# Performance work log

Hardware: AMD Instinct MI355X
Metric: run time of the kernel (lower is better)

## Reference

```python
import jax, jax.numpy as jnp
import numpy as np

D = 256; H = 8; L = 4; P = 4; DFF = 1024
B = 4; NQ = 900
SHAPES = np.array([[100, 160], [50, 80], [25, 40], [13, 20]], dtype=np.int64)
NV = int((SHAPES[:, 0] * SHAPES[:, 1]).sum())


def setup_inputs():
    key = jax.random.key(0)
    ks = jax.random.split(key, 16)
    def w(k, shape):
        return jax.random.normal(k, shape, jnp.float32) * 0.02
    return {
        "tgt": jax.random.normal(ks[0], (B, NQ, D), jnp.float32),
        "tgt_query_pos": jax.random.normal(ks[1], (B, NQ, D), jnp.float32),
        "tgt_reference_points": jax.random.uniform(ks[2], (B, NQ, L, 2), dtype=jnp.float32),
        "memory": jax.random.normal(ks[3], (B, NV, D), jnp.float32),
        "value_proj_w": w(ks[4], (D, D)), "value_proj_b": jnp.zeros((D,), jnp.float32),
        "samp_off_w": w(ks[5], (H * L * P * 2, D)), "samp_off_b": jnp.zeros((H * L * P * 2,), jnp.float32),
        "attn_w_w": w(ks[6], (H * L * P, D)), "attn_w_b": jnp.zeros((H * L * P,), jnp.float32),
        "ca_out_w": w(ks[7], (D, D)), "ca_out_b": jnp.zeros((D,), jnp.float32),
        "ln1_g": jnp.ones((D,), jnp.float32), "ln1_b": jnp.zeros((D,), jnp.float32),
        "in_proj_w": w(ks[8], (3 * D, D)), "in_proj_b": jnp.zeros((3 * D,), jnp.float32),
        "sa_out_w": w(ks[9], (D, D)), "sa_out_b": jnp.zeros((D,), jnp.float32),
        "ln2_g": jnp.ones((D,), jnp.float32), "ln2_b": jnp.zeros((D,), jnp.float32),
        "ffn1_w": w(ks[10], (DFF, D)), "ffn1_b": jnp.zeros((DFF,), jnp.float32),
        "ffn2_w": w(ks[11], (D, DFF)), "ffn2_b": jnp.zeros((D,), jnp.float32),
        "ln3_g": jnp.ones((D,), jnp.float32), "ln3_b": jnp.zeros((D,), jnp.float32),
        "spatial_shapes": jnp.asarray(SHAPES),
    }


def layer_norm(x, g, b, eps=1e-5):
    m = x.mean(-1, keepdims=True)
    v = ((x - m) ** 2).mean(-1, keepdims=True)
    return (x - m) / jnp.sqrt(v + eps) * g + b


def ms_deform_attn(query, refp, value, shapes, Wv, bv, Wo, bo, Wa, ba, Wout, bout):
    # query [B,Nq,D], refp [B,Nq,L,2] in [0,1], value [B,NV,D]; shapes: np [L,2] (H,W)
    Bq, Nq, Dm = query.shape
    dh = Dm // H
    v = (value @ Wv.T + bv).reshape(Bq, -1, H, dh)
    off = (query @ Wo.T + bo).reshape(Bq, Nq, H, L, P, 2)
    aw = jax.nn.softmax((query @ Wa.T + ba).reshape(Bq, Nq, H, L * P), axis=-1)
    aw = aw.reshape(Bq, Nq, H, L, P)
    norm = jnp.asarray(np.stack([shapes[:, 1], shapes[:, 0]], -1), jnp.float32)  # [L,2] = (W,H)
    loc = refp[:, :, None, :, None, :] + off / norm[None, None, None, :, None, :]  # [B,Nq,H,L,P,2]
    starts = np.concatenate([[0], np.cumsum(shapes[:, 0] * shapes[:, 1])])
    acc = jnp.zeros((Bq, Nq, H, dh), query.dtype)
    for l in range(L):
        Hl, Wl = int(shapes[l, 0]), int(shapes[l, 1])
        vf = v[:, int(starts[l]):int(starts[l]) + Hl * Wl]                 # [B,HW,H,dh]
        v2 = vf.transpose(0, 2, 1, 3).reshape(Bq * H, Hl * Wl, dh)
        # grid_sample align_corners=False: pixel = loc*size - 0.5
        xl = loc[:, :, :, l, :, 0] * Wl - 0.5                              # [B,Nq,H,P]
        yl = loc[:, :, :, l, :, 1] * Hl - 0.5
        x0 = jnp.floor(xl); y0 = jnp.floor(yl)
        wx = xl - x0; wy = yl - y0
        x0i = x0.astype(jnp.int32); y0i = y0.astype(jnp.int32)
        def corner(xi, yi, wgt):
            valid = (xi >= 0) & (xi < Wl) & (yi >= 0) & (yi < Hl)
            idx = jnp.clip(yi, 0, Hl - 1) * Wl + jnp.clip(xi, 0, Wl - 1)   # [B,Nq,H,P]
            idx2 = idx.transpose(0, 2, 1, 3).reshape(Bq * H, Nq * P)
            g = jnp.take_along_axis(v2, idx2[..., None], axis=1)           # [B*H,Nq*P,dh]
            g = g.reshape(Bq, H, Nq, P, dh).transpose(0, 2, 1, 3, 4)
            return g * (wgt * valid).astype(query.dtype)[..., None]
        s = (corner(x0i, y0i, (1 - wx) * (1 - wy))
             + corner(x0i + 1, y0i, wx * (1 - wy))
             + corner(x0i, y0i + 1, (1 - wx) * wy)
             + corner(x0i + 1, y0i + 1, wx * wy))                          # [B,Nq,H,P,dh]
        acc = acc + jnp.einsum('bqhpd,bqhp->bqhd', s, aw[:, :, :, l])
    return acc.reshape(Bq, Nq, Dm) @ Wout.T + bout


def mha(q, k, v, Win, bin_, Wout, bout):
    Dm = q.shape[-1]; dh = Dm // H
    def proj(x, W, b):
        return (x @ W.T + b).reshape(x.shape[0], x.shape[1], H, dh)
    qh = proj(q, Win[:Dm], bin_[:Dm])
    kh = proj(k, Win[Dm:2 * Dm], bin_[Dm:2 * Dm])
    vh = proj(v, Win[2 * Dm:], bin_[2 * Dm:])
    att = jax.nn.softmax(jnp.einsum('bqhd,bkhd->bhqk', qh, kh) / np.sqrt(dh).astype(np.float32), axis=-1)
    o = jnp.einsum('bhqk,bkhd->bqhd', att, vh).reshape(q.shape[0], q.shape[1], Dm)
    return o @ Wout.T + bout


def _forward(tgt, tgt_query_pos, tgt_reference_points, memory,
             value_proj_w, value_proj_b, samp_off_w, samp_off_b, attn_w_w, attn_w_b,
             ca_out_w, ca_out_b, ln1_g, ln1_b, in_proj_w, in_proj_b, sa_out_w, sa_out_b,
             ln2_g, ln2_b, ffn1_w, ffn1_b, ffn2_w, ffn2_b, ln3_g, ln3_b, shapes):
    # cross (deformable) attention
    q = tgt + tgt_query_pos
    tgt2 = ms_deform_attn(q, tgt_reference_points, memory, shapes,
                          value_proj_w, value_proj_b, samp_off_w, samp_off_b,
                          attn_w_w, attn_w_b, ca_out_w, ca_out_b)
    x = layer_norm(tgt + tgt2, ln1_g, ln1_b)
    # self attention (q=k=x+pos, v=x)
    qk = x + tgt_query_pos
    x = layer_norm(x + mha(qk, qk, x, in_proj_w, in_proj_b, sa_out_w, sa_out_b), ln2_g, ln2_b)
    # FFN
    ff = jax.nn.relu(x @ ffn1_w.T + ffn1_b) @ ffn2_w.T + ffn2_b
    return layer_norm(x + ff, ln3_g, ln3_b)


def reference(tgt, tgt_query_pos, tgt_reference_points, memory,
              value_proj_w, value_proj_b, samp_off_w, samp_off_b, attn_w_w, attn_w_b,
              ca_out_w, ca_out_b, ln1_g, ln1_b, in_proj_w, in_proj_b, sa_out_w, sa_out_b,
              ln2_g, ln2_b, ffn1_w, ffn1_b, ffn2_w, ffn2_b, ln3_g, ln3_b, spatial_shapes):
    shapes = np.asarray(spatial_shapes)
    return _forward(tgt, tgt_query_pos, tgt_reference_points, memory,
                    value_proj_w, value_proj_b, samp_off_w, samp_off_b, attn_w_w, attn_w_b,
                    ca_out_w, ca_out_b, ln1_g, ln1_b, in_proj_w, in_proj_b, sa_out_w, sa_out_b,
                    ln2_g, ln2_b, ffn1_w, ffn1_b, ffn2_w, ffn2_b, ln3_g, ln3_b, shapes)
```

## Files before the change

kernel.cpp:

```cpp
#include <hip/hip_runtime.h>

constexpr int D_   = 256;
constexpr int H_   = 8;
constexpr int DH   = 32;
constexpr int L_   = 4;
constexpr int P_   = 4;
constexpr int DFF_ = 1024;
constexpr int B_   = 4;
constexpr int NQ_  = 900;
constexpr int NV_  = 21260;
constexpr int MQ   = B_ * NQ_;
constexpr int MV   = B_ * NV_;

typedef __attribute__((ext_vector_type(8))) short short8;
typedef __attribute__((ext_vector_type(4))) float f32x4;

static __device__ __forceinline__ unsigned short f2bf(float x) {
  union { float f; unsigned int u; } v;
  v.f = x;
  const unsigned int r = v.u + 0x7fffu + ((v.u >> 16) & 1u);
  return (unsigned short)(r >> 16);
}
static __device__ __forceinline__ float bf2f(unsigned short u) {
  union { unsigned int i; float f; } x;
  x.i = ((unsigned int)u) << 16;
  return x.f;
}

struct CvtArgs {
  const float* src[9];
  unsigned short* dst[9];
  int n[9];
  float scl[9];
};

__global__ __launch_bounds__(256) void cvtw(CvtArgs a) {
  const int seg = blockIdx.y;
  const int n = a.n[seg];
  const float s = a.scl[seg];
  const float* __restrict__ sp = a.src[seg];
  unsigned short* __restrict__ d = a.dst[seg];
  for (int i = (blockIdx.x * 256 + threadIdx.x) * 4; i < n;
       i += gridDim.x * 256 * 4) {
    const float4 v = *reinterpret_cast<const float4*>(&sp[i]);
    d[i + 0] = f2bf(v.x * s); d[i + 1] = f2bf(v.y * s);
    d[i + 2] = f2bf(v.z * s); d[i + 3] = f2bf(v.w * s);
  }
}

__global__ void biasprep(const float* __restrict__ bin,
                         const float* __restrict__ bo,
                         const float* __restrict__ ba,
                         float* __restrict__ bqkv, float* __restrict__ bfu) {
  const int i = threadIdx.x;
  if (i < 768) bqkv[i] = (i < 256) ? bin[i] * 0.17677669529663687f : bin[i];
  if (i < 384) bfu[i] = (i < 256) ? bo[i] : ba[i - 256];
}

template <bool ABF, bool ADD2, bool RELU, bool OUTBF>
__global__ __launch_bounds__(256) void gemm_db(
    const void* __restrict__ Ap, const float* __restrict__ A2,
    const unsigned short* __restrict__ Wbf, const float* __restrict__ bias,
    void* __restrict__ Cp, int M, int N, int K) {
  constexpr int LDR = 40;
  __shared__ unsigned short As[2][128][LDR];
  __shared__ unsigned short Bs[2][128][LDR];

  const float* Af = (const float*)Ap;
  const unsigned short* Ab = (const unsigned short*)Ap;
  float* Cf = (float*)Cp;
  unsigned short* Cb = (unsigned short*)Cp;

  const int t    = threadIdx.x;
  const int wave = t >> 6;
  const int l    = t & 63;
  const int n0   = blockIdx.x * 128;
  const int m0   = blockIdx.y * 128;
  const int wm   = (wave >> 1) * 64;
  const int wn   = (wave & 1) * 64;
  const int srow = t >> 1;
  const int sseg = (t & 1) * 16;
  const int lr   = l & 15;
  const int lk   = (l >> 4) * 8;

  const int am = m0 + srow;
  const bool aok = am < M;
  const size_t arow = (size_t)am * K;
  const size_t brow = (size_t)(n0 + srow) * K;

  f32x4 acc[4][4];
#pragma unroll
  for (int i = 0; i < 4; ++i)
#pragma unroll
    for (int j = 0; j < 4; ++j) acc[i][j] = (f32x4)0.f;

  short8 ar0, ar1, br0, br1;

  auto LOAD = [&](int k0) {
    if constexpr (ABF) {
      if (aok) {
        ar0 = *reinterpret_cast<const short8*>(&Ab[arow + k0 + sseg]);
        ar1 = *reinterpret_cast<const short8*>(&Ab[arow + k0 + sseg + 8]);
      } else {
        ar0 = (short8)(short)0; ar1 = (short8)(short)0;
      }
    } else {
      if (aok) {
        float f[16];
#pragma unroll
        for (int j = 0; j < 4; ++j) {
          const float4 av =
              *reinterpret_cast<const float4*>(&Af[arow + k0 + sseg + 4 * j]);
          f[4 * j + 0] = av.x; f[4 * j + 1] = av.y;
          f[4 * j + 2] = av.z; f[4 * j + 3] = av.w;
        }
        if constexpr (ADD2) {
#pragma unroll
          for (int j = 0; j < 4; ++j) {
            const float4 av =
                *reinterpret_cast<const float4*>(&A2[arow + k0 + sseg + 4 * j]);
            f[4 * j + 0] += av.x; f[4 * j + 1] += av.y;
            f[4 * j + 2] += av.z; f[4 * j + 3] += av.w;
          }
        }
        alignas(16) unsigned short u[16];
#pragma unroll
        for (int j = 0; j < 16; ++j) u[j] = f2bf(f[j]);
        ar0 = *reinterpret_cast<short8*>(&u[0]);
        ar1 = *reinterpret_cast<short8*>(&u[8]);
      } else {
        ar0 = (short8)(short)0; ar1 = (short8)(short)0;
      }
    }
    br0 = *reinterpret_cast<const short8*>(&Wbf[brow + k0 + sseg]);
    br1 = *reinterpret_cast<const short8*>(&Wbf[brow + k0 + sseg + 8]);
  };

  const int nt = K >> 5;
  LOAD(0);
  for (int tt = 0; tt < nt; ++tt) {
    const int cur = tt & 1;
    *reinterpret_cast<short8*>(&As[cur][srow][sseg])     = ar0;
    *reinterpret_cast<short8*>(&As[cur][srow][sseg + 8]) = ar1;
    *reinterpret_cast<short8*>(&Bs[cur][srow][sseg])     = br0;
    *reinterpret_cast<short8*>(&Bs[cur][srow][sseg + 8]) = br1;
    if (tt + 1 < nt) LOAD((tt + 1) << 5);
    __syncthreads();

    short8 af[4], bfr[4];
#pragma unroll
    for (int fi = 0; fi < 4; ++fi)
      af[fi] = *reinterpret_cast<const short8*>(&As[cur][wm + fi * 16 + lr][lk]);
#pragma unroll
    for (int fj = 0; fj < 4; ++fj)
      bfr[fj] = *reinterpret_cast<const short8*>(&Bs[cur][wn + fj * 16 + lr][lk]);

#pragma unroll
    for (int fi = 0; fi < 4; ++fi)
#pragma unroll
      for (int fj = 0; fj < 4; ++fj)
        acc[fi][fj] = __builtin_amdgcn_mfma_f32_16x16x32_bf16(
            af[fi], bfr[fj], acc[fi][fj], 0, 0, 0);
  }

  const int orow = (l >> 4) * 4;
#pragma unroll
  for (int fi = 0; fi < 4; ++fi) {
#pragma unroll
    for (int fj = 0; fj < 4; ++fj) {
      const int n = n0 + wn + fj * 16 + lr;
      const float bn = bias[n];
#pragma unroll
      for (int i = 0; i < 4; ++i) {
        const int m = m0 + wm + fi * 16 + orow + i;
        if (m < M) {
          float vv = acc[fi][fj][i] + bn;
          if (RELU) vv = fmaxf(vv, 0.f);
          if (OUTBF)
            Cb[(size_t)m * N + n] = f2bf(vv);
          else
            Cf[(size_t)m * N + n] = vv;
        }
      }
    }
  }
}

template <int K, bool ABF, bool ADD2, bool RELU, bool OUTBF>
__global__ __launch_bounds__(256) void gemm_p2(
    const void* __restrict__ Ap, const float* __restrict__ A2,
    const unsigned short* __restrict__ Wbf, const float* __restrict__ bias,
    void* __restrict__ Cp, int M, int N) {
  constexpr int LDR = 40;
  constexpr int NT = K / 32;
  __shared__ unsigned short As[2][128][LDR];
  __shared__ unsigned short Bs[2][128][LDR];

  const float* Af = (const float*)Ap;
  const unsigned short* Ab = (const unsigned short*)Ap;
  float* Cf = (float*)Cp;
  unsigned short* Cb = (unsigned short*)Cp;

  const int t    = threadIdx.x;
  const int wave = t >> 6;
  const int l    = t & 63;
  const int n0   = blockIdx.x * 128;
  const int m0   = blockIdx.y * 128;
  const int wm   = (wave >> 1) * 64;
  const int wn   = (wave & 1) * 64;
  const int srow = t >> 1;
  const int sseg = (t & 1) * 16;
  const int lr   = l & 15;
  const int lk   = (l >> 4) * 8;

  const int am = m0 + srow;
  const bool aok = am < M;
  const size_t arow = (size_t)am * K;
  const size_t brow = (size_t)(n0 + srow) * K;

  f32x4 acc[4][4];
#pragma unroll
  for (int i = 0; i < 4; ++i)
#pragma unroll
    for (int j = 0; j < 4; ++j) acc[i][j] = (f32x4)0.f;

  float  frA[16], frB[16];
  short8 abA0, abA1, abB0, abB1;
  short8 brA0, brA1, brB0, brB1;

#define LOAD_SLOT(SUF, k0)                                                     \
  do {                                                                         \
    if constexpr (ABF) {                                                       \
      if (aok) {                                                               \
        ab##SUF##0 = *reinterpret_cast<const short8*>(&Ab[arow + (k0) + sseg]);\
        ab##SUF##1 = *reinterpret_cast<const short8*>(&Ab[arow + (k0) + sseg + 8]);\
      } else {                                                                 \
        ab##SUF##0 = (short8)(short)0; ab##SUF##1 = (short8)(short)0;          \
      }                                                                        \
    } else {                                                                   \
      if (aok) {                                                               \
        _Pragma("unroll")                                                      \
        for (int j = 0; j < 4; ++j) {                                          \
          const float4 av =                                                    \
              *reinterpret_cast<const float4*>(&Af[arow + (k0) + sseg + 4 * j]);\
          fr##SUF[4 * j + 0] = av.x; fr##SUF[4 * j + 1] = av.y;                \
          fr##SUF[4 * j + 2] = av.z; fr##SUF[4 * j + 3] = av.w;                \
        }                                                                      \
        if constexpr (ADD2) {                                                  \
          _Pragma("unroll")                                                    \
          for (int j = 0; j < 4; ++j) {                                        \
            const float4 av =                                                  \
                *reinterpret_cast<const float4*>(&A2[arow + (k0) + sseg + 4 * j]);\
            fr##SUF[4 * j + 0] += av.x; fr##SUF[4 * j + 1] += av.y;            \
            fr##SUF[4 * j + 2] += av.z; fr##SUF[4 * j + 3] += av.w;            \
          }                                                                    \
        }                                                                      \
      } else {                                                                 \
        _Pragma("unroll")                                                      \
        for (int j = 0; j < 16; ++j) fr##SUF[j] = 0.f;                         \
      }                                                                        \
    }                                                                          \
    br##SUF##0 = *reinterpret_cast<const short8*>(&Wbf[brow + (k0) + sseg]);   \
    br##SUF##1 = *reinterpret_cast<const short8*>(&Wbf[brow + (k0) + sseg + 8]);\
  } while (0)

#define WRITE_SLOT(SUF, BUF)                                                   \
  do {                                                                         \
    if constexpr (ABF) {                                                       \
      *reinterpret_cast<short8*>(&As[BUF][srow][sseg])     = ab##SUF##0;       \
      *reinterpret_cast<short8*>(&As[BUF][srow][sseg + 8]) = ab##SUF##1;       \
    } else {                                                                   \
      alignas(16) unsigned short u[16];                                        \
      _Pragma("unroll")                                                        \
      for (int j = 0; j < 16; ++j) u[j] = f2bf(fr##SUF[j]);                    \
      *reinterpret_cast<short8*>(&As[BUF][srow][sseg]) =                       \
          *reinterpret_cast<short8*>(&u[0]);                                   \
      *reinterpret_cast<short8*>(&As[BUF][srow][sseg + 8]) =                   \
          *reinterpret_cast<short8*>(&u[8]);                                   \
    }                                                                          \
    *reinterpret_cast<short8*>(&Bs[BUF][srow][sseg])     = br##SUF##0;         \
    *reinterpret_cast<short8*>(&Bs[BUF][srow][sseg + 8]) = br##SUF##1;         \
  } while (0)

#define MFMA_STEP(BUF)                                                         \
  do {                                                                         \
    short8 af0 = *reinterpret_cast<const short8*>(&As[BUF][wm +  0 + lr][lk]); \
    short8 af1 = *reinterpret_cast<const short8*>(&As[BUF][wm + 16 + lr][lk]); \
    short8 af2 = *reinterpret_cast<const short8*>(&As[BUF][wm + 32 + lr][lk]); \
    short8 af3 = *reinterpret_cast<const short8*>(&As[BUF][wm + 48 + lr][lk]); \
    short8 bf0 = *reinterpret_cast<const short8*>(&Bs[BUF][wn +  0 + lr][lk]); \
    short8 bf1 = *reinterpret_cast<const short8*>(&Bs[BUF][wn + 16 + lr][lk]); \
    short8 bf2 = *reinterpret_cast<const short8*>(&Bs[BUF][wn + 32 + lr][lk]); \
    short8 bf3 = *reinterpret_cast<const short8*>(&Bs[BUF][wn + 48 + lr][lk]); \
    acc[0][0] = __builtin_amdgcn_mfma_f32_16x16x32_bf16(af0, bf0, acc[0][0], 0, 0, 0); \
    acc[0][1] = __builtin_amdgcn_mfma_f32_16x16x32_bf16(af0, bf1, acc[0][1], 0, 0, 0); \
    acc[0][2] = __builtin_amdgcn_mfma_f32_16x16x32_bf16(af0, bf2, acc[0][2], 0, 0, 0); \
    acc[0][3] = __builtin_amdgcn_mfma_f32_16x16x32_bf16(af0, bf3, acc[0][3], 0, 0, 0); \
    acc[1][0] = __builtin_amdgcn_mfma_f32_16x16x32_bf16(af1, bf0, acc[1][0], 0, 0, 0); \
    acc[1][1] = __builtin_amdgcn_mfma_f32_16x16x32_bf16(af1, bf1, acc[1][1], 0, 0, 0); \
    acc[1][2] = __builtin_amdgcn_mfma_f32_16x16x32_bf16(af1, bf2, acc[1][2], 0, 0, 0); \
    acc[1][3] = __builtin_amdgcn_mfma_f32_16x16x32_bf16(af1, bf3, acc[1][3], 0, 0, 0); \
    acc[2][0] = __builtin_amdgcn_mfma_f32_16x16x32_bf16(af2, bf0, acc[2][0], 0, 0, 0); \
    acc[2][1] = __builtin_amdgcn_mfma_f32_16x16x32_bf16(af2, bf1, acc[2][1], 0, 0, 0); \
    acc[2][2] = __builtin_amdgcn_mfma_f32_16x16x32_bf16(af2, bf2, acc[2][2], 0, 0, 0); \
    acc[2][3] = __builtin_amdgcn_mfma_f32_16x16x32_bf16(af2, bf3, acc[2][3], 0, 0, 0); \
    acc[3][0] = __builtin_amdgcn_mfma_f32_16x16x32_bf16(af3, bf0, acc[3][0], 0, 0, 0); \
    acc[3][1] = __builtin_amdgcn_mfma_f32_16x16x32_bf16(af3, bf1, acc[3][1], 0, 0, 0); \
    acc[3][2] = __builtin_amdgcn_mfma_f32_16x16x32_bf16(af3, bf2, acc[3][2], 0, 0, 0); \
    acc[3][3] = __builtin_amdgcn_mfma_f32_16x16x32_bf16(af3, bf3, acc[3][3], 0, 0, 0); \
  } while (0)

  LOAD_SLOT(A, 0);
  LOAD_SLOT(B, 32);
#pragma unroll
  for (int tt = 0; tt < NT; tt += 2) {
    WRITE_SLOT(A, 0);
    if (tt + 2 < NT) LOAD_SLOT(A, (tt + 2) * 32);
    __syncthreads();
    MFMA_STEP(0);

    WRITE_SLOT(B, 1);
    if (tt + 3 < NT) LOAD_SLOT(B, (tt + 3) * 32);
    __syncthreads();
    MFMA_STEP(1);
  }
#undef LOAD_SLOT
#undef WRITE_SLOT
#undef MFMA_STEP

  const int orow = (l >> 4) * 4;
#pragma unroll
  for (int fi = 0; fi < 4; ++fi) {
#pragma unroll
    for (int fj = 0; fj < 4; ++fj) {
      const int n = n0 + wn + fj * 16 + lr;
      const float bn = bias[n];
#pragma unroll
      for (int i = 0; i < 4; ++i) {
        const int m = m0 + wm + fi * 16 + orow + i;
        if (m < M) {
          float vv = acc[fi][fj][i] + bn;
          if (RELU) vv = fmaxf(vv, 0.f);
          if (OUTBF)
            Cb[(size_t)m * N + n] = f2bf(vv);
          else
            Cf[(size_t)m * N + n] = vv;
        }
      }
    }
  }
}

template <bool ABF, bool ADD2, bool RELU, bool OUTBF>
__global__ __launch_bounds__(256) void gemm_bres(
    const void* __restrict__ Ap, const float* __restrict__ A2,
    const unsigned short* __restrict__ Wbf, const float* __restrict__ bias,
    void* __restrict__ Cp, int M, int N, int add_nlim) {
  __shared__ unsigned short Bs[32768];
  __shared__ unsigned short As[2][64][40];

  const float* Af = (const float*)Ap;
  const unsigned short* Ab = (const unsigned short*)Ap;
  float* Cf = (float*)Cp;
  unsigned short* Cb = (unsigned short*)Cp;

  const int t    = threadIdx.x;
  const int wave = t >> 6;
  const int l    = t & 63;
  const int n0   = blockIdx.x * 128;
  const int m0   = blockIdx.y * 64;
  const int wm   = (wave >> 1) * 32;
  const int wcg  = (wave & 1) * 4;
  const int lr   = l & 15;
  const int lk8  = (l >> 4) * 8;
  const bool doadd = ADD2 && (n0 < add_nlim);

#pragma unroll
  for (int i = 0; i < 16; ++i) {
    const int e  = i * 256 + t;
    const int el = e & 63;
    const int cg = (e >> 6) & 7;
    const int st = e >> 9;
    const int row = n0 + cg * 16 + (el & 15);
    const int col = st * 32 + ((el >> 4) * 8);
    *reinterpret_cast<short8*>(&Bs[e * 8]) =
        *reinterpret_cast<const short8*>(&Wbf[(size_t)row * 256 + col]);
  }

  const int arow = t >> 2;
  const int acol = (t & 3) * 8;
  const int am   = m0 + arow;
  const bool aok = am < M;
  const size_t abase = (size_t)am * 256 + acol;

  float  fr[3][8];
  short8 br_[3];

  auto ALOAD = [&](int slot, int tt) {
    const int k0 = tt * 32;
    if constexpr (ABF) {
      br_[slot] = aok ? *reinterpret_cast<const short8*>(&Ab[abase + k0])
                      : (short8)(short)0;
    } else {
      if (aok) {
        const float4 a0 = *reinterpret_cast<const float4*>(&Af[abase + k0]);
        const float4 a1 = *reinterpret_cast<const float4*>(&Af[abase + k0 + 4]);
        fr[slot][0] = a0.x; fr[slot][1] = a0.y;
        fr[slot][2] = a0.z; fr[slot][3] = a0.w;
        fr[slot][4] = a1.x; fr[slot][5] = a1.y;
        fr[slot][6] = a1.z; fr[slot][7] = a1.w;
        if constexpr (ADD2) {
          if (doadd) {
            const float4 b0 = *reinterpret_cast<const float4*>(&A2[abase + k0]);
            const float4 b1 = *reinterpret_cast<const float4*>(&A2[abase + k0 + 4]);
            fr[slot][0] += b0.x; fr[slot][1] += b0.y;
            fr[slot][2] += b0.z; fr[slot][3] += b0.w;
            fr[slot][4] += b1.x; fr[slot][5] += b1.y;
            fr[slot][6] += b1.z; fr[slot][7] += b1.w;
          }
        }
      } else {
#pragma unroll
        for (int j = 0; j < 8; ++j) fr[slot][j] = 0.f;
      }
    }
  };
  auto AWRITE = [&](int slot, int tt) {
    if constexpr (ABF) {
      *reinterpret_cast<short8*>(&As[tt & 1][arow][acol]) = br_[slot];
    } else {
      alignas(16) unsigned short u[8];
#pragma unroll
      for (int j = 0; j < 8; ++j) u[j] = f2bf(fr[slot][j]);
      *reinterpret_cast<short8*>(&As[tt & 1][arow][acol]) =
          *reinterpret_cast<short8*>(&u[0]);
    }
  };

  f32x4 acc[2][4];
#pragma unroll
  for (int fi = 0; fi < 2; ++fi)
#pragma unroll
    for (int fj = 0; fj < 4; ++fj) acc[fi][fj] = (f32x4)0.f;

  ALOAD(0, 0); ALOAD(1, 1); ALOAD(2, 2);

#pragma unroll
  for (int tt = 0; tt < 8; ++tt) {
    AWRITE(tt % 3, tt);
    if (tt + 3 < 8) ALOAD(tt % 3, tt + 3);
    __syncthreads();

    short8 afr[2];
#pragma unroll
    for (int fi = 0; fi < 2; ++fi)
      afr[fi] = *reinterpret_cast<const short8*>(&As[tt & 1][wm + fi * 16 + lr][lk8]);

#pragma unroll
    for (int fj = 0; fj < 4; ++fj) {
      const short8 bfr = *reinterpret_cast<const short8*>(
          &Bs[(((tt * 8) + wcg + fj) * 64 + l) * 8]);
      acc[0][fj] = __builtin_amdgcn_mfma_f32_16x16x32_bf16(afr[0], bfr, acc[0][fj], 0, 0, 0);
      acc[1][fj] = __builtin_amdgcn_mfma_f32_16x16x32_bf16(afr[1], bfr, acc[1][fj], 0, 0, 0);
    }
  }

  const int or4 = (l >> 4) * 4;
#pragma unroll
  for (int fi = 0; fi < 2; ++fi) {
#pragma unroll
    for (int fj = 0; fj < 4; ++fj) {
      const int n = n0 + (wave & 1) * 64 + fj * 16 + lr;
      const float bn = bias[n];
#pragma unroll
      for (int i = 0; i < 4; ++i) {
        const int m = m0 + wm + fi * 16 + or4 + i;
        if (m < M) {
          float vv = acc[fi][fj][i] + bn;
          if (RELU) vv = fmaxf(vv, 0.f);
          if (OUTBF)
            Cb[(size_t)m * N + n] = f2bf(vv);
          else
            Cf[(size_t)m * N + n] = vv;
        }
      }
    }
  }
}

__global__ __launch_bounds__(256) void deform(const float* __restrict__ refp,
                                              const float* __restrict__ offlog,
                                              const unsigned short* __restrict__ v,
                                              unsigned int* __restrict__ accb2) {
  __shared__ float aw[2][128];
  const int t  = threadIdx.x;
  const int tq = t >> 7;
  const int tt = t & 127;
  const int bq = blockIdx.x * 2 + tq;
  const int b  = bq / NQ_;
  const int h  = tt >> 4;
  const int dd = tt & 15;

  aw[tq][tt] = offlog[(size_t)bq * 384 + 256 + tt];
  __syncthreads();
  if (t < 16) {
    const int q = t >> 3, hh = t & 7;
    float* a = &aw[q][hh * 16];
    float mx = -1e30f;
#pragma unroll
    for (int i = 0; i < 16; ++i) mx = fmaxf(mx, a[i]);
    float e[16], s = 0.f;
#pragma unroll
    for (int i = 0; i < 16; ++i) { e[i] = expf(a[i] - mx); s += e[i]; }
    const float inv = 1.f / s;
#pragma unroll
    for (int i = 0; i < 16; ++i) a[i] = e[i] * inv;
  }
  __syncthreads();

  constexpr int ST[4] = {0, 16000, 20000, 21000};
  constexpr int HL[4] = {100, 50, 25, 13};
  constexpr int WL[4] = {160, 80, 40, 20};

  float a0 = 0.f, a1 = 0.f;
#pragma unroll
  for (int l = 0; l < L_; ++l) {
    const float rx = refp[(bq * L_ + l) * 2 + 0];
    const float ry = refp[(bq * L_ + l) * 2 + 1];
    const float Wf = (float)WL[l], Hf = (float)HL[l];
    const int   Wi = WL[l], Hi = HL[l];
    const size_t vbase = (size_t)(b * NV_ + ST[l]) * D_ + h * DH + dd * 2;
#pragma unroll
    for (int p = 0; p < P_; ++p) {
      const float ox = offlog[(size_t)bq * 384 + h * 32 + l * 8 + p * 2 + 0];
      const float oy = offlog[(size_t)bq * 384 + h * 32 + l * 8 + p * 2 + 1];
      const float locx = rx + ox / Wf;
      const float locy = ry + oy / Hf;
      const float xl = locx * Wf - 0.5f;
      const float yl = locy * Hf - 0.5f;
      const float x0 = floorf(xl), y0 = floorf(yl);
      const float wx = xl - x0, wy = yl - y0;
      const int x0i = (int)x0, y0i = (int)y0;
      const float w = aw[tq][h * 16 + l * 4 + p];

      float s0 = 0.f, s1 = 0.f;
#pragma unroll
      for (int c = 0; c < 4; ++c) {
        const int xi = x0i + (c & 1);
        const int yi = y0i + (c >> 1);
        const float cw = ((c & 1) ? wx : 1.f - wx) * ((c >> 1) ? wy : 1.f - wy);
        const bool valid = (xi >= 0) && (xi < Wi) && (yi >= 0) && (yi < Hi);
        const int xc = min(max(xi, 0), Wi - 1);
        const int yc = min(max(yi, 0), Hi - 1);
        const unsigned int g2 = *reinterpret_cast<const unsigned int*>(
            &v[vbase + (size_t)(yc * Wi + xc) * D_]);
        const float g0 = bf2f((unsigned short)(g2 & 0xffffu));
        const float g1 = bf2f((unsigned short)(g2 >> 16));
        s0 += valid ? g0 * cw : 0.f;
        s1 += valid ? g1 * cw : 0.f;
      }
      a0 += w * s0;
      a1 += w * s1;
    }
  }
  const unsigned int packed =
      (unsigned int)f2bf(a0) | ((unsigned int)f2bf(a1) << 16);
  accb2[((size_t)bq * D_ + h * DH + dd * 2) >> 1] = packed;
}

constexpr int TQM  = 64;
constexpr int NQTM = (NQ_ + TQM - 1) / TQM;

__global__ __launch_bounds__(256) void mha_mfma(
    const unsigned short* __restrict__ qkvh,
    unsigned short* __restrict__ o) {
  __shared__ unsigned short Qs[64][40];
  __shared__ unsigned short Ks[64][40];
  __shared__ unsigned short Vts[32][72];
  __shared__ unsigned short Ps[64][72];

  const int bx = blockIdx.x;
  const int qt = bx % NQTM;
  const int h  = (bx / NQTM) % H_;
  const int b  = bx / (NQTM * H_);
  const int t  = threadIdx.x;
  const int wave = t >> 6;
  const int l    = t & 63;
  const int q0   = qt * TQM;
  const int wrow = wave * 16;
  const int lr   = l & 15;
  const int lkb  = (l >> 4) * 8;

  const int kr = t >> 2, kcb = (t & 3) * 8;
  const int vk = t & 63, vdb = (t >> 6) * 8;

  short8 ku, vu;
  auto LOADKV = [&](int kt) {
    const int k0 = kt * 64;
    const int nk = min(64, NQ_ - k0);
    ku = (kr < nk) ? *reinterpret_cast<const short8*>(
                         &qkvh[(size_t)(b * NQ_ + k0 + kr) * 768 + 256 + h * DH + kcb])
                   : (short8)(short)0;
    vu = (vk < nk) ? *reinterpret_cast<const short8*>(
                         &qkvh[(size_t)(b * NQ_ + k0 + vk) * 768 + 512 + h * DH + vdb])
                   : (short8)(short)0;
  };

  {
    short8 u;
    if (q0 + kr < NQ_)
      u = *reinterpret_cast<const short8*>(
          &qkvh[(size_t)(b * NQ_ + q0 + kr) * 768 + h * DH + kcb]);
    else
      u = (short8)(short)0;
    *reinterpret_cast<short8*>(&Qs[kr][kcb]) = u;
  }
  LOADKV(0);
  __syncthreads();

  const short8 qa = *reinterpret_cast<const short8*>(&Qs[wrow + lr][lkb]);

  f32x4 oacc[2];
  oacc[0] = (f32x4)0.f; oacc[1] = (f32x4)0.f;
  float m_[4] = {-1e30f, -1e30f, -1e30f, -1e30f};
  float l_[4] = {0.f, 0.f, 0.f, 0.f};

  for (int kt = 0; kt < NQTM; ++kt) {
    const int k0 = kt * 64;
    const int nk = min(64, NQ_ - k0);
    __syncthreads();

    *reinterpret_cast<short8*>(&Ks[kr][kcb]) = ku;
#pragma unroll
    for (int j = 0; j < 8; ++j) Vts[vdb + j][vk] = (unsigned short)vu[j];

    if (kt + 1 < NQTM) LOADKV(kt + 1);
    __syncthreads();

    f32x4 sacc[4];
#pragma unroll
    for (int fj = 0; fj < 4; ++fj)
      sacc[fj] = __builtin_amdgcn_mfma_f32_16x16x32_bf16(
          qa, *reinterpret_cast<const short8*>(&Ks[16 * fj + lr][lkb]),
          (f32x4)0.f, 0, 0, 0);

    bool cv[4];
#pragma unroll
    for (int fj = 0; fj < 4; ++fj) cv[fj] = (16 * fj + lr) < nk;

    float p0[4], p1[4], p2[4], p3[4], sc_[4];
#pragma unroll
    for (int i = 0; i < 4; ++i) {
      float tm = -1e30f;
      if (cv[0]) tm = fmaxf(tm, sacc[0][i]);
      if (cv[1]) tm = fmaxf(tm, sacc[1][i]);
      if (cv[2]) tm = fmaxf(tm, sacc[2][i]);
      if (cv[3]) tm = fmaxf(tm, sacc[3][i]);
      tm = fmaxf(tm, __shfl_xor(tm, 1));
      tm = fmaxf(tm, __shfl_xor(tm, 2));
      tm = fmaxf(tm, __shfl_xor(tm, 4));
      tm = fmaxf(tm, __shfl_xor(tm, 8));
      const float mn = fmaxf(m_[i], tm);
      sc_[i] = __expf(m_[i] - mn);
      m_[i] = mn;
      const float e0 = cv[0] ? __expf(sacc[0][i] - mn) : 0.f;
      const float e1 = cv[1] ? __expf(sacc[1][i] - mn) : 0.f;
      const float e2 = cv[2] ? __expf(sacc[2][i] - mn) : 0.f;
      const float e3 = cv[3] ? __expf(sacc[3][i] - mn) : 0.f;
      p0[i] = e0; p1[i] = e1; p2[i] = e2; p3[i] = e3;
      float rs = e0 + e1 + e2 + e3;
      rs += __shfl_xor(rs, 1);
      rs += __shfl_xor(rs, 2);
      rs += __shfl_xor(rs, 4);
      rs += __shfl_xor(rs, 8);
      l_[i] = l_[i] * sc_[i] + rs;
    }

#pragma unroll
    for (int i = 0; i < 4; ++i) {
      const int pr = wrow + (l >> 4) * 4 + i;
      Ps[pr][0  + lr] = f2bf(p0[i]);
      Ps[pr][16 + lr] = f2bf(p1[i]);
      Ps[pr][32 + lr] = f2bf(p2[i]);
      Ps[pr][48 + lr] = f2bf(p3[i]);
    }

    const short8 pa0 = *reinterpret_cast<const short8*>(&Ps[wrow + lr][lkb]);
    const short8 pa1 = *reinterpret_cast<const short8*>(&Ps[wrow + lr][lkb + 32]);
#pragma unroll
    for (int nt = 0; nt < 2; ++nt) {
      f32x4 c = oacc[nt];
#pragma unroll
      for (int i = 0; i < 4; ++i) c[i] *= sc_[i];
      c = __builtin_amdgcn_mfma_f32_16x16x32_bf16(
          pa0, *reinterpret_cast<const short8*>(&Vts[16 * nt + lr][lkb]), c, 0, 0, 0);
      c = __builtin_amdgcn_mfma_f32_16x16x32_bf16(
          pa1, *reinterpret_cast<const short8*>(&Vts[16 * nt + lr][lkb + 32]), c, 0, 0, 0);
      oacc[nt] = c;
    }
  }

#pragma unroll
  for (int i = 0; i < 4; ++i) {
    const int r = (l >> 4) * 4 + i;
    const int q = q0 + wrow + r;
    if (q < NQ_) {
      const float inv = 1.f / l_[i];
      o[(size_t)(b * NQ_ + q) * D_ + h * DH + 0  + lr] = f2bf(oacc[0][i] * inv);
      o[(size_t)(b * NQ_ + q) * D_ + h * DH + 16 + lr] = f2bf(oacc[1][i] * inv);
    }
  }
}

__global__ __launch_bounds__(256) void ln4(const float* __restrict__ res,
                                           const float* __restrict__ add,
                                           const float* __restrict__ g,
                                           const float* __restrict__ bt,
                                           float* __restrict__ out) {
  const int wave = threadIdx.x >> 6, lane = threadIdx.x & 63;
  const int r = blockIdx.x * 4 + wave;
  const size_t base = (size_t)r * D_ + lane * 4;
  const float4 a = *reinterpret_cast<const float4*>(&res[base]);
  const float4 bv = *reinterpret_cast<const float4*>(&add[base]);
  float4 x;
  x.x = a.x + bv.x; x.y = a.y + bv.y; x.z = a.z + bv.z; x.w = a.w + bv.w;

  float s = x.x + x.y + x.z + x.w;
#pragma unroll
  for (int off = 1; off < 64; off <<= 1) s += __shfl_xor(s, off);
  const float mean = s * (1.f / D_);

  const float dx0 = x.x - mean, dx1 = x.y - mean, dx2 = x.z - mean,
              dx3 = x.w - mean;
  float v = dx0 * dx0 + dx1 * dx1 + dx2 * dx2 + dx3 * dx3;
#pragma unroll
  for (int off = 1; off < 64; off <<= 1) v += __shfl_xor(v, off);
  const float rstd = rsqrtf(v * (1.f / D_) + 1e-5f);

  const float4 gg = *reinterpret_cast<const float4*>(&g[lane * 4]);
  const float4 bb = *reinterpret_cast<const float4*>(&bt[lane * 4]);
  float4 o;
  o.x = dx0 * rstd * gg.x + bb.x;
  o.y = dx1 * rstd * gg.y + bb.y;
  o.z = dx2 * rstd * gg.z + bb.z;
  o.w = dx3 * rstd * gg.w + bb.w;
  *reinterpret_cast<float4*>(&out[base]) = o;
}

extern "C" void kernel_launch(void* const* d_in, const int* in_sizes, int n_in,
                              void* d_out, int out_size, void* d_ws,
                              size_t ws_size, hipStream_t stream) {
  const float* tgt   = (const float*)d_in[0];
  const float* pos   = (const float*)d_in[1];
  const float* refp  = (const float*)d_in[2];
  const float* mem   = (const float*)d_in[3];
  const float* Wv    = (const float*)d_in[4];
  const float* bv    = (const float*)d_in[5];
  const float* Wo    = (const float*)d_in[6];
  const float* bo    = (const float*)d_in[7];
  const float* Wa    = (const float*)d_in[8];
  const float* ba    = (const float*)d_in[9];
  const float* Wca   = (const float*)d_in[10];
  const float* bca   = (const float*)d_in[11];
  const float* g1    = (const float*)d_in[12];
  const float* b1    = (const float*)d_in[13];
  const float* Win   = (const float*)d_in[14];
  const float* bin   = (const float*)d_in[15];
  const float* Wsa   = (const float*)d_in[16];
  const float* bsa   = (const float*)d_in[17];
  const float* g2    = (const float*)d_in[18];
  const float* b2    = (const float*)d_in[19];
  const float* W1    = (const float*)d_in[20];
  const float* bb1   = (const float*)d_in[21];
  const float* W2    = (const float*)d_in[22];
  const float* bb2   = (const float*)d_in[23];
  const float* g3    = (const float*)d_in[24];
  const float* b3    = (const float*)d_in[25];

  char* cur = (char*)d_ws;
  auto alloc = [&](size_t bytes) {
    char* p = cur;
    cur += (bytes + 255) & ~(size_t)255;
    return (void*)p;
  };
  unsigned short* v_bf    = (unsigned short*)alloc((size_t)MV * 256 * 2);
  float*          offlog  = (float*)alloc((size_t)MQ * 384 * 4);
  unsigned short* accb_bf = (unsigned short*)alloc((size_t)MQ * 256 * 2);
  float*          tmp     = (float*)alloc((size_t)MQ * 256 * 4);
  float*          x1      = (float*)alloc((size_t)MQ * 256 * 4);
  float*          x2      = (float*)alloc((size_t)MQ * 256 * 4);
  unsigned short* qkvh_bf = (unsigned short*)alloc((size_t)MQ * 768 * 2);
  unsigned short* obuf_bf = (unsigned short*)alloc((size_t)MQ * 256 * 2);
  unsigned short* h1_bf   = (unsigned short*)alloc((size_t)MQ * 1024 * 2);
  unsigned short* Wv_bf   = (unsigned short*)alloc(65536 * 2);
  unsigned short* Wfu_bf  = (unsigned short*)alloc(98304 * 2);
  unsigned short* Wca_bf  = (unsigned short*)alloc(65536 * 2);
  unsigned short* Win_bf  = (unsigned short*)alloc(196608 * 2);
  unsigned short* Wsa_bf  = (unsigned short*)alloc(65536 * 2);
  unsigned short* W1_bf   = (unsigned short*)alloc(262144 * 2);
  unsigned short* W2_bf   = (unsigned short*)alloc(262144 * 2);
  float*          biasqkv = (float*)alloc(768 * 4);
  float*          bfused  = (float*)alloc(384 * 4);

  const float qscale = 0.17677669529663687f;

  CvtArgs ca;
  ca.src[0] = Wv;            ca.dst[0] = Wv_bf;          ca.n[0] = 65536;  ca.scl[0] = 1.f;
  ca.src[1] = Wo;            ca.dst[1] = Wfu_bf;         ca.n[1] = 65536;  ca.scl[1] = 1.f;
  ca.src[2] = Wa;            ca.dst[2] = Wfu_bf + 65536; ca.n[2] = 32768;  ca.scl[2] = 1.f;
  ca.src[3] = Wca;           ca.dst[3] = Wca_bf;         ca.n[3] = 65536;  ca.scl[3] = 1.f;
  ca.src[4] = Win;           ca.dst[4] = Win_bf;         ca.n[4] = 65536;  ca.scl[4] = qscale;
  ca.src[5] = Win + 65536;   ca.dst[5] = Win_bf + 65536; ca.n[5] = 131072; ca.scl[5] = 1.f;
  ca.src[6] = Wsa;           ca.dst[6] = Wsa_bf;         ca.n[6] = 65536;  ca.scl[6] = 1.f;
  ca.src[7] = W1;            ca.dst[7] = W1_bf;          ca.n[7] = 262144; ca.scl[7] = 1.f;
  ca.src[8] = W2;            ca.dst[8] = W2_bf;          ca.n[8] = 262144; ca.scl[8] = 1.f;
  cvtw<<<dim3(64, 9), 256, 0, stream>>>(ca);
  biasprep<<<1, 768, 0, stream>>>(bin, bo, ba, biasqkv, bfused);

  const int mqb64  = (MQ + 63) / 64;
  const int mvb128 = (MV + 127) / 128;

  gemm_db<false, false, false, true><<<dim3(2, mvb128), 256, 0, stream>>>(
      mem, nullptr, Wv_bf, bv, v_bf, MV, 256, 256);
  gemm_bres<false, true, false, false><<<dim3(3, mqb64), 256, 0, stream>>>(
      tgt, pos, Wfu_bf, bfused, offlog, MQ, 384, 384);
  deform<<<MQ / 2, 256, 0, stream>>>(refp, offlog, v_bf,
                                     (unsigned int*)accb_bf);
  gemm_bres<true, false, false, false><<<dim3(2, mqb64), 256, 0, stream>>>(
      accb_bf, nullptr, Wca_bf, bca, tmp, MQ, 256, 0);
  ln4<<<MQ / 4, 256, 0, stream>>>(tgt, tmp, g1, b1, x1);
  gemm_bres<false, true, false, true><<<dim3(6, mqb64), 256, 0, stream>>>(
      x1, pos, Win_bf, biasqkv, qkvh_bf, MQ, 768, 512);
  mha_mfma<<<B_ * H_ * NQTM, 256, 0, stream>>>(qkvh_bf, obuf_bf);
  gemm_bres<true, false, false, false><<<dim3(2, mqb64), 256, 0, stream>>>(
      obuf_bf, nullptr, Wsa_bf, bsa, tmp, MQ, 256, 0);
  ln4<<<MQ / 4, 256, 0, stream>>>(x1, tmp, g2, b2, x2);
  gemm_bres<false, false, true, true><<<dim3(8, mqb64), 256, 0, stream>>>(
      x2, nullptr, W1_bf, bb1, h1_bf, MQ, 1024, 0);
  gemm_p2<1024, true, false, false, false><<<dim3(2, (MQ + 127) / 128), 256, 0, stream>>>(
      h1_bf, nullptr, W2_bf, bb2, tmp, MQ, 256);
  ln4<<<MQ / 4, 256, 0, stream>>>(x2, tmp, g3, b3, (float*)d_out);
}
```

Baseline: 201.1 us.

## Split-K FFN2 GEMM with LDS-resident weights and remap deform block order

Result: faster. 193.6 us, median of 2 (-3.7%).

```diff
diff --git a/kernel.cpp b/kernel.cpp
--- a/kernel.cpp
+++ b/kernel.cpp
@@ -162,171 +162,6 @@
         acc[fi][fj] = __builtin_amdgcn_mfma_f32_16x16x32_bf16(
             af[fi], bfr[fj], acc[fi][fj], 0, 0, 0);
   }
-
-  const int orow = (l >> 4) * 4;
-#pragma unroll
-  for (int fi = 0; fi < 4; ++fi) {
-#pragma unroll
-    for (int fj = 0; fj < 4; ++fj) {
-      const int n = n0 + wn + fj * 16 + lr;
-      const float bn = bias[n];
-#pragma unroll
-      for (int i = 0; i < 4; ++i) {
-        const int m = m0 + wm + fi * 16 + orow + i;
-        if (m < M) {
-          float vv = acc[fi][fj][i] + bn;
-          if (RELU) vv = fmaxf(vv, 0.f);
-          if (OUTBF)
-            Cb[(size_t)m * N + n] = f2bf(vv);
-          else
-            Cf[(size_t)m * N + n] = vv;
-        }
-      }
-    }
-  }
-}
-
-template <int K, bool ABF, bool ADD2, bool RELU, bool OUTBF>
-__global__ __launch_bounds__(256) void gemm_p2(
-    const void* __restrict__ Ap, const float* __restrict__ A2,
-    const unsigned short* __restrict__ Wbf, const float* __restrict__ bias,
-    void* __restrict__ Cp, int M, int N) {
-  constexpr int LDR = 40;
-  constexpr int NT = K / 32;
-  __shared__ unsigned short As[2][128][LDR];
-  __shared__ unsigned short Bs[2][128][LDR];
-
-  const float* Af = (const float*)Ap;
-  const unsigned short* Ab = (const unsigned short*)Ap;
-  float* Cf = (float*)Cp;
-  unsigned short* Cb = (unsigned short*)Cp;
-
-  const int t    = threadIdx.x;
-  const int wave = t >> 6;
-  const int l    = t & 63;
-  const int n0   = blockIdx.x * 128;
-  const int m0   = blockIdx.y * 128;
-  const int wm   = (wave >> 1) * 64;
-  const int wn   = (wave & 1) * 64;
-  const int srow = t >> 1;
-  const int sseg = (t & 1) * 16;
-  const int lr   = l & 15;
-  const int lk   = (l >> 4) * 8;
-
-  const int am = m0 + srow;
-  const bool aok = am < M;
-  const size_t arow = (size_t)am * K;
-  const size_t brow = (size_t)(n0 + srow) * K;
-
-  f32x4 acc[4][4];
-#pragma unroll
-  for (int i = 0; i < 4; ++i)
-#pragma unroll
-    for (int j = 0; j < 4; ++j) acc[i][j] = (f32x4)0.f;
-
-  float  frA[16], frB[16];
-  short8 abA0, abA1, abB0, abB1;
-  short8 brA0, brA1, brB0, brB1;
-
-#define LOAD_SLOT(SUF, k0)                                                     \
-  do {                                                                         \
-    if constexpr (ABF) {                                                       \
-      if (aok) {                                                               \
-        ab##SUF##0 = *reinterpret_cast<const short8*>(&Ab[arow + (k0) + sseg]);\
-        ab##SUF##1 = *reinterpret_cast<const short8*>(&Ab[arow + (k0) + sseg + 8]);\
-      } else {                                                                 \
-        ab##SUF##0 = (short8)(short)0; ab##SUF##1 = (short8)(short)0;          \
-      }                                                                        \
-    } else {                                                                   \
-      if (aok) {                                                               \
-        _Pragma("unroll")                                                      \
-        for (int j = 0; j < 4; ++j) {                                          \
-          const float4 av =                                                    \
-              *reinterpret_cast<const float4*>(&Af[arow + (k0) + sseg + 4 * j]);\
-          fr##SUF[4 * j + 0] = av.x; fr##SUF[4 * j + 1] = av.y;                \
-          fr##SUF[4 * j + 2] = av.z; fr##SUF[4 * j + 3] = av.w;                \
-        }                                                                      \
-        if constexpr (ADD2) {                                                  \
-          _Pragma("unroll")                                                    \
-          for (int j = 0; j < 4; ++j) {                                        \
-            const float4 av =                                                  \
-                *reinterpret_cast<const float4*>(&A2[arow + (k0) + sseg + 4 * j]);\
-            fr##SUF[4 * j + 0] += av.x; fr##SUF[4 * j + 1] += av.y;            \
-            fr##SUF[4 * j + 2] += av.z; fr##SUF[4 * j + 3] += av.w;            \
-          }                                                                    \
-        }                                                                      \
-      } else {                                                                 \
-        _Pragma("unroll")                                                      \
-        for (int j = 0; j < 16; ++j) fr##SUF[j] = 0.f;                         \
-      }                                                                        \
-    }                                                                          \
-    br##SUF##0 = *reinterpret_cast<const short8*>(&Wbf[brow + (k0) + sseg]);   \
-    br##SUF##1 = *reinterpret_cast<const short8*>(&Wbf[brow + (k0) + sseg + 8]);\
-  } while (0)
-
-#define WRITE_SLOT(SUF, BUF)                                                   \
-  do {                                                                         \
-    if constexpr (ABF) {                                                       \
-      *reinterpret_cast<short8*>(&As[BUF][srow][sseg])     = ab##SUF##0;       \
-      *reinterpret_cast<short8*>(&As[BUF][srow][sseg + 8]) = ab##SUF##1;       \
-    } else {                                                                   \
-      alignas(16) unsigned short u[16];                                        \
-      _Pragma("unroll")                                                        \
-      for (int j = 0; j < 16; ++j) u[j] = f2bf(fr##SUF[j]);                    \
-      *reinterpret_cast<short8*>(&As[BUF][srow][sseg]) =                       \
-          *reinterpret_cast<short8*>(&u[0]);                                   \
-      *reinterpret_cast<short8*>(&As[BUF][srow][sseg + 8]) =                   \
-          *reinterpret_cast<short8*>(&u[8]);                                   \
-    }                                                                          \
-    *reinterpret_cast<short8*>(&Bs[BUF][srow][sseg])     = br##SUF##0;         \
-    *reinterpret_cast<short8*>(&Bs[BUF][srow][sseg + 8]) = br##SUF##1;         \
-  } while (0)
-
-#define MFMA_STEP(BUF)                                                         \
-  do {                                                                         \
-    short8 af0 = *reinterpret_cast<const short8*>(&As[BUF][wm +  0 + lr][lk]); \
-    short8 af1 = *reinterpret_cast<const short8*>(&As[BUF][wm + 16 + lr][lk]); \
-    short8 af2 = *reinterpret_cast<const short8*>(&As[BUF][wm + 32 + lr][lk]); \
-    short8 af3 = *reinterpret_cast<const short8*>(&As[BUF][wm + 48 + lr][lk]); \
-    short8 bf0 = *reinterpret_cast<const short8*>(&Bs[BUF][wn +  0 + lr][lk]); \
-    short8 bf1 = *reinterpret_cast<const short8*>(&Bs[BUF][wn + 16 + lr][lk]); \
-    short8 bf2 = *reinterpret_cast<const short8*>(&Bs[BUF][wn + 32 + lr][lk]); \
-    short8 bf3 = *reinterpret_cast<const short8*>(&Bs[BUF][wn + 48 + lr][lk]); \
-    acc[0][0] = __builtin_amdgcn_mfma_f32_16x16x32_bf16(af0, bf0, acc[0][0], 0, 0, 0); \
-    acc[0][1] = __builtin_amdgcn_mfma_f32_16x16x32_bf16(af0, bf1, acc[0][1], 0, 0, 0); \
-    acc[0][2] = __builtin_amdgcn_mfma_f32_16x16x32_bf16(af0, bf2, acc[0][2], 0, 0, 0); \
-    acc[0][3] = __builtin_amdgcn_mfma_f32_16x16x32_bf16(af0, bf3, acc[0][3], 0, 0, 0); \
-    acc[1][0] = __builtin_amdgcn_mfma_f32_16x16x32_bf16(af1, bf0, acc[1][0], 0, 0, 0); \
-    acc[1][1] = __builtin_amdgcn_mfma_f32_16x16x32_bf16(af1, bf1, acc[1][1], 0, 0, 0); \
-    acc[1][2] = __builtin_amdgcn_mfma_f32_16x16x32_bf16(af1, bf2, acc[1][2], 0, 0, 0); \
-    acc[1][3] = __builtin_amdgcn_mfma_f32_16x16x32_bf16(af1, bf3, acc[1][3], 0, 0, 0); \
-    acc[2][0] = __builtin_amdgcn_mfma_f32_16x16x32_bf16(af2, bf0, acc[2][0], 0, 0, 0); \
-    acc[2][1] = __builtin_amdgcn_mfma_f32_16x16x32_bf16(af2, bf1, acc[2][1], 0, 0, 0); \
-    acc[2][2] = __builtin_amdgcn_mfma_f32_16x16x32_bf16(af2, bf2, acc[2][2], 0, 0, 0); \
-    acc[2][3] = __builtin_amdgcn_mfma_f32_16x16x32_bf16(af2, bf3, acc[2][3], 0, 0, 0); \
-    acc[3][0] = __builtin_amdgcn_mfma_f32_16x16x32_bf16(af3, bf0, acc[3][0], 0, 0, 0); \
-    acc[3][1] = __builtin_amdgcn_mfma_f32_16x16x32_bf16(af3, bf1, acc[3][1], 0, 0, 0); \
-    acc[3][2] = __builtin_amdgcn_mfma_f32_16x16x32_bf16(af3, bf2, acc[3][2], 0, 0, 0); \
-    acc[3][3] = __builtin_amdgcn_mfma_f32_16x16x32_bf16(af3, bf3, acc[3][3], 0, 0, 0); \
-  } while (0)
-
-  LOAD_SLOT(A, 0);
-  LOAD_SLOT(B, 32);
-#pragma unroll
-  for (int tt = 0; tt < NT; tt += 2) {
-    WRITE_SLOT(A, 0);
-    if (tt + 2 < NT) LOAD_SLOT(A, (tt + 2) * 32);
-    __syncthreads();
-    MFMA_STEP(0);
-
-    WRITE_SLOT(B, 1);
-    if (tt + 3 < NT) LOAD_SLOT(B, (tt + 3) * 32);
-    __syncthreads();
-    MFMA_STEP(1);
-  }
-#undef LOAD_SLOT
-#undef WRITE_SLOT
-#undef MFMA_STEP
 
   const int orow = (l >> 4) * 4;
 #pragma unroll
@@ -488,15 +323,126 @@
   }
 }
 
+__global__ __launch_bounds__(256) void gemm_ffn2(
+    const unsigned short* __restrict__ Ab,
+    const unsigned short* __restrict__ Wbf,
+    float* __restrict__ Cpart, int M) {
+  __shared__ unsigned short Bs[32768];
+  __shared__ unsigned short As[2][64][40];
+
+  const int t    = threadIdx.x;
+  const int wave = t >> 6;
+  const int l    = t & 63;
+  const int n0   = blockIdx.x * 128;
+  const int m0   = blockIdx.y * 64;
+  const int kz   = blockIdx.z * 256;
+  const int wm   = (wave >> 1) * 32;
+  const int wcg  = (wave & 1) * 4;
+  const int lr   = l & 15;
+  const int lk8  = (l >> 4) * 8;
+
+#pragma unroll
+  for (int i = 0; i < 16; ++i) {
+    const int e  = i * 256 + t;
+    const int el = e & 63;
+    const int cg = (e >> 6) & 7;
+    const int st = e >> 9;
+    const int row = n0 + cg * 16 + (el & 15);
+    const int col = kz + st * 32 + ((el >> 4) * 8);
+    *reinterpret_cast<short8*>(&Bs[e * 8]) =
+        *reinterpret_cast<const short8*>(&Wbf[(size_t)row * 1024 + col]);
+  }
+
+  const int arow = t >> 2;
+  const int acol = (t & 3) * 8;
+  const int am   = m0 + arow;
+  const bool aok = am < M;
+  const size_t abase = (size_t)am * 1024 + kz + acol;
+
+  short8 br_[3];
+  auto ALOAD = [&](int slot, int tt) {
+    br_[slot] = aok ? *reinterpret_cast<const short8*>(&Ab[abase + tt * 32])
+                    : (short8)(short)0;
+  };
+  auto AWRITE = [&](int slot, int tt) {
+    *reinterpret_cast<short8*>(&As[tt & 1][arow][acol]) = br_[slot];
+  };
+
+  f32x4 acc[2][4];
+#pragma unroll
+  for (int fi = 0; fi < 2; ++fi)
+#pragma unroll
+    for (int fj = 0; fj < 4; ++fj) acc[fi][fj] = (f32x4)0.f;
+
+  ALOAD(0, 0); ALOAD(1, 1); ALOAD(2, 2);
+
+#pragma unroll
+  for (int tt = 0; tt < 8; ++tt) {
+    AWRITE(tt % 3, tt);
+    if (tt + 3 < 8) ALOAD(tt % 3, tt + 3);
+    __syncthreads();
+
+    short8 afr[2];
+#pragma unroll
+    for (int fi = 0; fi < 2; ++fi)
+      afr[fi] = *reinterpret_cast<const short8*>(&As[tt & 1][wm + fi * 16 + lr][lk8]);
+
+#pragma unroll
+    for (int fj = 0; fj < 4; ++fj) {
+      const short8 bfr = *reinterpret_cast<const short8*>(
+          &Bs[(((tt * 8) + wcg + fj) * 64 + l) * 8]);
+      acc[0][fj] = __builtin_amdgcn_mfma_f32_16x16x32_bf16(afr[0], bfr, acc[0][fj], 0, 0, 0);
+      acc[1][fj] = __builtin_amdgcn_mfma_f32_16x16x32_bf16(afr[1], bfr, acc[1][fj], 0, 0, 0);
+    }
+  }
+
+  float* out = &Cpart[(size_t)blockIdx.z * M * 256];
+  const int or4 = (l >> 4) * 4;
+#pragma unroll
+  for (int fi = 0; fi < 2; ++fi) {
+#pragma unroll
+    for (int fj = 0; fj < 4; ++fj) {
+      const int n = n0 + (wave & 1) * 64 + fj * 16 + lr;
+#pragma unroll
+      for (int i = 0; i < 4; ++i) {
+        const int m = m0 + wm + fi * 16 + or4 + i;
+        if (m < M) out[(size_t)m * 256 + n] = acc[fi][fj][i];
+      }
+    }
+  }
+}
+
+__global__ __launch_bounds__(256) void reduce4(const float* __restrict__ part,
+                                               const float* __restrict__ bias,
+                                               float* __restrict__ out, int M) {
+  const size_t i = ((size_t)blockIdx.x * 256 + threadIdx.x) * 4;
+  const size_t tot = (size_t)M * 256;
+  if (i >= tot) return;
+  const int nb = (int)(i & 255);
+  float4 s = *reinterpret_cast<const float4*>(&part[i]);
+  const float4 p1 = *reinterpret_cast<const float4*>(&part[tot + i]);
+  const float4 p2 = *reinterpret_cast<const float4*>(&part[2 * tot + i]);
+  const float4 p3 = *reinterpret_cast<const float4*>(&part[3 * tot + i]);
+  const float4 bb = *reinterpret_cast<const float4*>(&bias[nb]);
+  s.x += p1.x + p2.x + p3.x + bb.x;
+  s.y += p1.y + p2.y + p3.y + bb.y;
+  s.z += p1.z + p2.z + p3.z + bb.z;
+  s.w += p1.w + p2.w + p3.w + bb.w;
+  *reinterpret_cast<float4*>(&out[i]) = s;
+}
+
 __global__ __launch_bounds__(256) void deform(const float* __restrict__ refp,
                                               const float* __restrict__ offlog,
                                               const unsigned short* __restrict__ v,
                                               unsigned int* __restrict__ accb2) {
   __shared__ float aw[2][128];
+  const int nwg  = gridDim.x;
+  const int cpx  = nwg >> 3;
+  const int bidx = (blockIdx.x % 8) * cpx + blockIdx.x / 8;
   const int t  = threadIdx.x;
   const int tq = t >> 7;
   const int tt = t & 127;
-  const int bq = blockIdx.x * 2 + tq;
+  const int bq = bidx * 2 + tq;
   const int b  = bq / NQ_;
   const int h  = tt >> 4;
   const int dd = tt & 15;
@@ -792,6 +738,7 @@
   unsigned short* qkvh_bf = (unsigned short*)alloc((size_t)MQ * 768 * 2);
   unsigned short* obuf_bf = (unsigned short*)alloc((size_t)MQ * 256 * 2);
   unsigned short* h1_bf   = (unsigned short*)alloc((size_t)MQ * 1024 * 2);
+  float*          part    = (float*)alloc((size_t)4 * MQ * 256 * 4);
   unsigned short* Wv_bf   = (unsigned short*)alloc(65536 * 2);
   unsigned short* Wfu_bf  = (unsigned short*)alloc(98304 * 2);
   unsigned short* Wca_bf  = (unsigned short*)alloc(65536 * 2);
@@ -837,7 +784,7 @@
   ln4<<<MQ / 4, 256, 0, stream>>>(x1, tmp, g2, b2, x2);
   gemm_bres<false, false, true, true><<<dim3(8, mqb64), 256, 0, stream>>>(
       x2, nullptr, W1_bf, bb1, h1_bf, MQ, 1024, 0);
-  gemm_p2<1024, true, false, false, false><<<dim3(2, (MQ + 127) / 128), 256, 0, stream>>>(
-      h1_bf, nullptr, W2_bf, bb2, tmp, MQ, 256);
+  gemm_ffn2<<<dim3(2, mqb64, 4), 256, 0, stream>>>(h1_bf, W2_bf, part, MQ);
+  reduce4<<<(MQ * 256 / 4 + 255) / 256, 256, 0, stream>>>(part, bb2, tmp, MQ);
   ln4<<<MQ / 4, 256, 0, stream>>>(x2, tmp, g3, b3, (float*)d_out);
 }
```
